# Kernel optimization log

Hardware: AMD Instinct MI355X
Metric: run time of the kernel (lower is better)

The kernel has to match this reference:

```python
import jax, jax.numpy as jnp
import numpy as np

B, N, D_MODEL, N_HEADS, WINDOW = 2, 2048, 1024, 16, 512
HEAD_DIM = D_MODEL // N_HEADS

def setup_inputs() -> dict:
    key = jax.random.key(0)
    k1, k2, k3 = jax.random.split(key, 3)
    x = jax.random.normal(k1, (B, N, D_MODEL), dtype=jnp.float32)
    W_qkv = jax.random.normal(k2, (D_MODEL, 3 * D_MODEL), dtype=jnp.float32) * 0.02
    W_proj = jax.random.normal(k3, (D_MODEL, D_MODEL), dtype=jnp.float32) * 0.02
    b_proj = jnp.zeros((D_MODEL,), dtype=jnp.float32)
    return {"x": x, "W_qkv": W_qkv, "W_proj": W_proj, "b_proj": b_proj}

def reference(x, W_qkv, W_proj, b_proj):
    Bx, Nx, C = x.shape
    H, Dh = N_HEADS, C // N_HEADS
    scale = Dh ** -0.5
    window = min(WINDOW, Nx)
    half = window // 2
    # qkv: [B,N,3C] -> [3,B,H,N,Dh]
    qkv = (x @ W_qkv).reshape(Bx, Nx, 3, H, Dh).transpose(2, 0, 3, 1, 4)
    q, k, v = qkv[0], qkv[1], qkv[2]
    # banded mask: allowed iff i-half <= j <= i+half
    i = jnp.arange(Nx)[:, None]
    j = jnp.arange(Nx)[None, :]
    allowed = jnp.abs(i - j) <= half  # [N,N] bool
    attn = jnp.einsum('bhqd,bhkd->bhqk', q, k) * scale
    attn = jnp.where(allowed[None, None], attn, -jnp.inf)
    attn = jax.nn.softmax(attn, axis=-1)
    out = jnp.einsum('bhqk,bhkd->bhqd', attn, v)
    out = out.transpose(0, 2, 1, 3).reshape(Bx, Nx, C)
    return out @ W_proj + b_proj
```

## Files before the change

### kernel.cpp

```cpp
#include <hip/hip_runtime.h>
#include <stdint.h>


typedef _Float16 f16x8 __attribute__((ext_vector_type(8)));
typedef _Float16 f16x4 __attribute__((ext_vector_type(4)));
typedef float    f32x4 __attribute__((ext_vector_type(4)));

#define MFMA16(a, b, c) __builtin_amdgcn_mfma_f32_16x16x32_f16((a), (b), (c), 0, 0, 0)

__device__ __forceinline__ void gload16(const void* g, void* l) {
  __builtin_amdgcn_global_load_lds(
      (const __attribute__((address_space(1))) void*)g,
      (__attribute__((address_space(3))) void*)l, 16, 0, 0);
}

__global__ __launch_bounds__(256) void prep(const float* __restrict__ x,
                                            const float* __restrict__ wqkv,
                                            const float* __restrict__ wproj,
                                            _Float16* __restrict__ Xb,
                                            _Float16* __restrict__ Wqt,
                                            _Float16* __restrict__ Wpt) {
  __shared__ float t[64][65];
  const int id = blockIdx.x, tid = threadIdx.x;
  if (id < 4096) {
    int i = (id * 256 + tid) * 4;
    float4 v = *(const float4*)(x + i);
    f16x4 h;
    h[0] = (_Float16)v.x; h[1] = (_Float16)v.y;
    h[2] = (_Float16)v.z; h[3] = (_Float16)v.w;
    *(f16x4*)(Xb + i) = h;
    return;
  }
  const float* in; _Float16* out; int N, bx, by;
  if (id < 4864) { int tt = id - 4096; in = wqkv; out = Wqt; N = 3072; bx = tt % 48; by = tt / 48; }
  else           { int tt = id - 4864; in = wproj; out = Wpt; N = 1024; bx = tt & 15; by = tt >> 4; }
  const int n0 = bx * 64, k0 = by * 64;
  {
    int j = tid & 63;
#pragma unroll
    for (int p = 0; p < 16; p++) {
      int i = p * 4 + (tid >> 6);
      t[i][j] = in[(size_t)(k0 + i) * N + n0 + j];
    }
  }
  __syncthreads();
  {
    int i = tid & 63;
#pragma unroll
    for (int p = 0; p < 16; p++) {
      int j = p * 4 + (tid >> 6);
      out[(size_t)(n0 + j) * 1024 + k0 + i] = (_Float16)t[i][j];
    }
  }
}

__global__ __launch_bounds__(256) void vtrans(const _Float16* __restrict__ V,
                                              _Float16* __restrict__ Vt) {
  __shared__ _Float16 t[64][66];
  const int tid = threadIdx.x;
  const int bh = blockIdx.y, n0 = blockIdx.x * 64;
  const _Float16* Vg = V + (size_t)bh * 131072;
  {
    int dh0 = (tid & 7) * 8;
#pragma unroll
    for (int p = 0; p < 2; p++) {
      int nl = p * 32 + (tid >> 3);
      f16x8 v = *(const f16x8*)(Vg + (size_t)(n0 + nl) * 64 + dh0);
#pragma unroll
      for (int e = 0; e < 8; e++) t[nl][dh0 + e] = v[e];
    }
  }
  __syncthreads();
  {
    int dh = tid >> 2, nb = (tid & 3) * 16;
    f16x8 a, b;
#pragma unroll
    for (int e = 0; e < 8; e++) { a[e] = t[nb + e][dh]; b[e] = t[nb + 8 + e][dh]; }
    _Float16* dst = Vt + (size_t)bh * 131072 + (size_t)dh * 2048 + n0 + nb;
    *(f16x8*)dst = a;
    *(f16x8*)(dst + 8) = b;
  }
}

template <int BM, int BN, int EPI>
__global__ __launch_bounds__(256) void gemm16(const _Float16* __restrict__ A,
                                              const _Float16* __restrict__ Bt,
                                              const int K,
                                              _Float16* __restrict__ oh,
                                              float* __restrict__ of,
                                              const float* __restrict__ bias,
                                              const int Nout) {
  constexpr int RF = BM / 32, CF = BN / 32;
  constexpr int SLABS = (BM + BN) / 8;
  __shared__ __align__(16) char smem[(BM + BN) * 128];
  char* As = smem;
  char* Bs = smem + BM * 128;
  const int tid = threadIdx.x, wave = tid >> 6, lane = tid & 63;
  const int il = lane & 15, ih = lane >> 4;
  const int bm = blockIdx.y * BM, bn = blockIdx.x * BN;
  const int wm = wave >> 1, wn = wave & 1;
  const int rs = lane >> 3, cp = lane & 7;

  f32x4 acc[RF][CF] = {};

  for (int k0 = 0; k0 < K; k0 += 64) {
    __syncthreads();
#pragma unroll
    for (int s0 = 0; s0 < SLABS / 4; s0++) {
      int s = wave + s0 * 4;
      int row = s * 8 + rs;
      int c = cp ^ (row & 7);
      if (row < BM)
        gload16(A + (size_t)(bm + row) * K + k0 + c * 8, As + s * 1024);
      else
        gload16(Bt + (size_t)(bn + row - BM) * K + k0 + c * 8, smem + s * 1024);
    }
    __syncthreads();
#pragma unroll
    for (int ks = 0; ks < 2; ks++) {
      f16x8 af[RF], bf[CF];
#pragma unroll
      for (int rf = 0; rf < RF; rf++) {
        int R = wm * (BM / 2) + rf * 16 + il;
        af[rf] = *(const f16x8*)(As + R * 128 + (((ks * 4 + ih) ^ (R & 7)) * 16));
      }
#pragma unroll
      for (int cf = 0; cf < CF; cf++) {
        int C = wn * (BN / 2) + cf * 16 + il;
        bf[cf] = *(const f16x8*)(Bs + C * 128 + (((ks * 4 + ih) ^ (C & 7)) * 16));
      }
#pragma unroll
      for (int rf = 0; rf < RF; rf++)
#pragma unroll
        for (int cf = 0; cf < CF; cf++)
          acc[rf][cf] = MFMA16(af[rf], bf[cf], acc[rf][cf]);
    }
  }

#pragma unroll
  for (int rf = 0; rf < RF; rf++)
#pragma unroll
    for (int cf = 0; cf < CF; cf++)
#pragma unroll
      for (int r = 0; r < 4; r++) {
        int row = bm + wm * (BM / 2) + rf * 16 + ih * 4 + r;
        int col = bn + wn * (BN / 2) + cf * 16 + il;
        float v = acc[rf][cf][r];
        if (EPI == 0) {
          int sec = col >> 10, cc = col & 1023;
          if (sec == 0) v *= 0.18033688f;
          size_t plane = (size_t)(sec * 32 + (row >> 11) * 16 + (cc >> 6));
          oh[plane * 131072 + (size_t)(row & 2047) * 64 + (cc & 63)] = (_Float16)v;
        } else {
          of[(size_t)row * Nout + col] = v + bias[col];
        }
      }
}

__global__ __launch_bounds__(512) void attn128(const _Float16* __restrict__ QKV,
                                               const _Float16* __restrict__ VT,
                                               _Float16* __restrict__ O2) {
  __shared__ __align__(16) char smem[49152];
  const int tid = threadIdx.x, wave = tid >> 6, lane = tid & 63;
  const int il = lane & 15, ih = lane >> 4;
  const int q0 = blockIdx.x * 128, bh = blockIdx.y;
  const _Float16* Qg = QKV + (size_t)bh * 131072;
  const _Float16* Kg = QKV + 4194304 + (size_t)bh * 131072;
  const _Float16* Vg = VT + (size_t)bh * 131072;

  const int t0 = (q0 >= 256) ? (q0 - 256) : 0;
  const int t1 = (q0 + 384 <= 2048) ? (q0 + 384) : 2048;
  const int niter = (t1 - t0) >> 6;

  const int rs = lane >> 3, cp = lane & 7;
#pragma unroll
  for (int q = 0; q < 2; q++) {
    int s = wave * 2 + q;
    int row = s * 8 + rs;
    int c = cp ^ (row & 7);
    gload16(Qg + (size_t)(q0 + row) * 64 + c * 8, smem + s * 1024);
  }
  {
    char* Kp = smem + 16384;
    int row = wave * 8 + rs;
    int c = cp ^ (row & 7);
    gload16(Kg + (size_t)(t0 + row) * 64 + c * 8, Kp + wave * 1024);
    gload16(Vg + (size_t)row * 2048 + t0 + c * 8, Kp + 8192 + wave * 1024);
  }
  __syncthreads();

  f16x8 aq[2];
#pragma unroll
  for (int ks = 0; ks < 2; ks++) {
    int row = wave * 16 + il;
    aq[ks] = *(const f16x8*)(smem + row * 128 + (((ks * 4 + ih) ^ (row & 7)) * 16));
  }

  char* Pw = smem + wave * 2048;
  f32x4 o[4] = {};
  float l_r[4] = {0.f, 0.f, 0.f, 0.f};
  const int a0 = q0 + wave * 16;

  for (int i = 0; i < niter; i++) {
    const int kt = t0 + i * 64;
    char* Kp = smem + 16384 + (i & 1) * 16384;
    char* Vp = Kp + 8192;
    if (i + 1 < niter) {
      char* Kn = smem + 16384 + ((i + 1) & 1) * 16384;
      int kt2 = kt + 64;
      int row = wave * 8 + rs;
      int c = cp ^ (row & 7);
      gload16(Kg + (size_t)(kt2 + row) * 64 + c * 8, Kn + wave * 1024);
      gload16(Vg + (size_t)row * 2048 + kt2 + c * 8, Kn + 8192 + wave * 1024);
    }

    bool outb[4];
    int d0s[4];
#pragma unroll
    for (int cf = 0; cf < 4; cf++) {
      int d0 = a0 - (kt + cf * 16);
      d0s[cf] = d0;
      outb[cf] = (d0 >= 272) || (d0 <= -272);
    }
#pragma unroll
    for (int cf = 0; cf < 4; cf++) {
      if (outb[cf]) {
        if (!outb[cf ^ 1]) {
#pragma unroll
          for (int r = 0; r < 4; r++) {
            int prow = ih * 4 + r;
            int key = cf * 16 + il;
            *(_Float16*)(Pw + prow * 128 + (((key >> 3) ^ (prow & 7)) * 16) +
                         (key & 7) * 2) = (_Float16)0.f;
          }
        }
        continue;
      }
      f32x4 s4 = {0.f, 0.f, 0.f, 0.f};
#pragma unroll
      for (int ks = 0; ks < 2; ks++) {
        int kr = cf * 16 + il;
        f16x8 bk = *(const f16x8*)(Kp + kr * 128 + (((ks * 4 + ih) ^ (kr & 7)) * 16));
        s4 = MFMA16(aq[ks], bk, s4);
      }
      const int d0 = d0s[cf];
#pragma unroll
      for (int r = 0; r < 4; r++) {
        float p = __builtin_amdgcn_exp2f(s4[r]);
        int qr = ih * 4 + r;
        if (d0 == 256) p = (qr <= il) ? p : 0.f;
        else if (d0 == -256) p = (qr >= il) ? p : 0.f;
        l_r[r] += p;
        int key = cf * 16 + il;
        *(_Float16*)(Pw + qr * 128 + (((key >> 3) ^ (qr & 7)) * 16) +
                     (key & 7) * 2) = (_Float16)p;
      }
    }
#pragma unroll
    for (int ks = 0; ks < 2; ks++) {
      if (outb[2 * ks] && outb[2 * ks + 1]) continue;
      f16x8 pa = *(const f16x8*)(Pw + il * 128 + (((ks * 4 + ih) ^ (il & 7)) * 16));
#pragma unroll
      for (int f = 0; f < 4; f++) {
        int dr = f * 16 + il;
        f16x8 vb = *(const f16x8*)(Vp + dr * 128 + (((ks * 4 + ih) ^ (dr & 7)) * 16));
        o[f] = MFMA16(pa, vb, o[f]);
      }
    }
    __syncthreads();
  }

  const int b = bh >> 4, h = bh & 15;
#pragma unroll
  for (int r = 0; r < 4; r++) {
    float l = l_r[r];
    l += __shfl_xor(l, 1);
    l += __shfl_xor(l, 2);
    l += __shfl_xor(l, 4);
    l += __shfl_xor(l, 8);
    float inv = 1.0f / l;
    int n = a0 + ih * 4 + r;
#pragma unroll
    for (int f = 0; f < 4; f++) {
      int col = h * 64 + f * 16 + il;
      O2[(size_t)(b * 2048 + n) * 1024 + col] = (_Float16)(o[f][r] * inv);
    }
  }
}


extern "C" void kernel_launch(void* const* d_in, const int* in_sizes, int n_in,
                              void* d_out, int out_size, void* d_ws, size_t ws_size,
                              hipStream_t stream) {
  const float* x = (const float*)d_in[0];
  const float* wqkv = (const float*)d_in[1];
  const float* wproj = (const float*)d_in[2];
  const float* bproj = (const float*)d_in[3];
  float* out = (float*)d_out;
  char* ws = (char*)d_ws;

  _Float16* Xb  = (_Float16*)(ws);
  _Float16* Wqt = (_Float16*)(ws + (size_t)(8  << 20));
  _Float16* Wpt = (_Float16*)(ws + (size_t)(14 << 20));
  _Float16* QKV = (_Float16*)(ws + (size_t)(16 << 20));
  _Float16* Vt  = (_Float16*)(ws + (size_t)(40 << 20));
  _Float16* O2  = (_Float16*)(ws);

  prep<<<5120, 256, 0, stream>>>(x, wqkv, wproj, Xb, Wqt, Wpt);
  gemm16<128, 128, 0><<<dim3(24, 32), 256, 0, stream>>>(Xb, Wqt, 1024, QKV, nullptr,
                                                        nullptr, 0);
  vtrans<<<dim3(32, 32), 256, 0, stream>>>(QKV + 8388608, Vt);
  attn128<<<dim3(16, 32), 512, 0, stream>>>(QKV, Vt, O2);
  gemm16<128, 128, 1><<<dim3(8, 32), 256, 0, stream>>>(O2, Wpt, 1024, nullptr, out,
                                                       bproj, 1024);
}
```

Before: 169.4 us.

## Restructure banded attention with 32x32 MFMA and split-key waves

The attention kernel now uses 32x32x16 MFMA tiles. Each pair of waves shares 32 query rows and splits each 128-key tile between them, and the two partial outputs are merged through shared memory at the end. K/V double buffering is replaced by a single 128-key buffer that is loaded after a barrier, trading prefetch overlap for fewer loop iterations and larger MFMA tiles. The output projection GEMM also switches to 128x64 tiles, doubling the block count to improve occupancy.

```diff
diff --git a/kernel.cpp b/kernel.cpp
--- a/kernel.cpp
+++ b/kernel.cpp
@@ -5,8 +5,10 @@
 typedef _Float16 f16x8 __attribute__((ext_vector_type(8)));
 typedef _Float16 f16x4 __attribute__((ext_vector_type(4)));
 typedef float    f32x4 __attribute__((ext_vector_type(4)));
+typedef float    f32x16 __attribute__((ext_vector_type(16)));
 
 #define MFMA16(a, b, c) __builtin_amdgcn_mfma_f32_16x16x32_f16((a), (b), (c), 0, 0, 0)
+#define MFMA32(a, b, c) __builtin_amdgcn_mfma_f32_32x32x16_f16((a), (b), (c), 0, 0, 0)
 
 __device__ __forceinline__ void gload16(const void* g, void* l) {
   __builtin_amdgcn_global_load_lds(
@@ -157,134 +159,155 @@
       }
 }
 
-__global__ __launch_bounds__(512) void attn128(const _Float16* __restrict__ QKV,
-                                               const _Float16* __restrict__ VT,
-                                               _Float16* __restrict__ O2) {
-  __shared__ __align__(16) char smem[49152];
+__global__ __launch_bounds__(512) void attn(const _Float16* __restrict__ QKV,
+                                            const _Float16* __restrict__ VT,
+                                            _Float16* __restrict__ O2) {
+  __shared__ __align__(16) char smem[65536];
+  char* Ks = smem + 32768;
+  char* Vs = smem + 49152;
   const int tid = threadIdx.x, wave = tid >> 6, lane = tid & 63;
-  const int il = lane & 15, ih = lane >> 4;
+  const int qw = wave >> 1, sh = wave & 1;
+  const int cl = lane & 31, hl = lane >> 5;
+  const int rs = lane >> 3, cp = lane & 7;
   const int q0 = blockIdx.x * 128, bh = blockIdx.y;
   const _Float16* Qg = QKV + (size_t)bh * 131072;
   const _Float16* Kg = QKV + 4194304 + (size_t)bh * 131072;
   const _Float16* Vg = VT + (size_t)bh * 131072;
-
-  const int t0 = (q0 >= 256) ? (q0 - 256) : 0;
-  const int t1 = (q0 + 384 <= 2048) ? (q0 + 384) : 2048;
-  const int niter = (t1 - t0) >> 6;
-
-  const int rs = lane >> 3, cp = lane & 7;
+  const int t0 = (q0 >= 256) ? q0 - 256 : 0;
+  const int t1 = (q0 + 384 <= 2048) ? q0 + 384 : 2048;
+  const int niter = (t1 - t0) >> 7;
+
 #pragma unroll
   for (int q = 0; q < 2; q++) {
-    int s = wave * 2 + q;
+    int s = 2 * wave + q;
     int row = s * 8 + rs;
     int c = cp ^ (row & 7);
     gload16(Qg + (size_t)(q0 + row) * 64 + c * 8, smem + s * 1024);
   }
-  {
-    char* Kp = smem + 16384;
-    int row = wave * 8 + rs;
-    int c = cp ^ (row & 7);
-    gload16(Kg + (size_t)(t0 + row) * 64 + c * 8, Kp + wave * 1024);
-    gload16(Vg + (size_t)row * 2048 + t0 + c * 8, Kp + 8192 + wave * 1024);
-  }
-  __syncthreads();
-
-  f16x8 aq[2];
-#pragma unroll
-  for (int ks = 0; ks < 2; ks++) {
-    int row = wave * 16 + il;
-    aq[ks] = *(const f16x8*)(smem + row * 128 + (((ks * 4 + ih) ^ (row & 7)) * 16));
-  }
-
-  char* Pw = smem + wave * 2048;
-  f32x4 o[4] = {};
-  float l_r[4] = {0.f, 0.f, 0.f, 0.f};
-  const int a0 = q0 + wave * 16;
+#pragma unroll
+  for (int q = 0; q < 2; q++) {
+    int s = 2 * wave + q;
+    int krow = s * 8 + rs;
+    int c = cp ^ (krow & 7);
+    gload16(Kg + (size_t)(t0 + krow) * 64 + c * 8, Ks + s * 1024);
+    int sub = s >> 3, vrow = (s & 7) * 8 + rs;
+    int cv = cp ^ (vrow & 7);
+    gload16(Vg + (size_t)vrow * 2048 + t0 + 64 * sub + cv * 8,
+            Vs + sub * 8192 + (s & 7) * 1024);
+  }
+  __syncthreads();
+  f16x8 bq[4];
+  {
+    int row = 32 * qw + cl;
+#pragma unroll
+    for (int ks = 0; ks < 4; ks++)
+      bq[ks] = *(const f16x8*)(smem + row * 128 + (((ks * 2 + hl) ^ (row & 7)) * 16));
+  }
+  __syncthreads();
+
+  char* Pw = smem + wave * 4096;
+  f32x16 oacc[2] = {};
+  float l_acc = 0.f;
+  const int a0 = q0 + 32 * qw;
 
   for (int i = 0; i < niter; i++) {
-    const int kt = t0 + i * 64;
-    char* Kp = smem + 16384 + (i & 1) * 16384;
-    char* Vp = Kp + 8192;
+    const int kt = t0 + i * 128;
+    const int d0a = a0 - (kt + 64 * sh);
+    const int d0b = d0a - 32;
+    const bool deadA = (d0a >= 288) || (d0a <= -288);
+    const bool deadB = (d0b >= 288) || (d0b <= -288);
+    if (!(deadA && deadB)) {
+#pragma unroll
+      for (int cb = 0; cb < 2; cb++) {
+        const int d0 = cb ? d0b : d0a;
+        const bool dead = cb ? deadB : deadA;
+        if (dead) {
+#pragma unroll
+          for (int g = 0; g < 4; g++) {
+            f16x4 z = {};
+            *(f16x4*)(Pw + cl * 128 + (((4 * cb + g) ^ (cl & 7)) * 16) + 8 * hl) = z;
+          }
+          continue;
+        }
+        f32x16 st = {};
+        const int krow = 64 * sh + 32 * cb + cl;
+#pragma unroll
+        for (int ks = 0; ks < 4; ks++) {
+          f16x8 ak = *(const f16x8*)(Ks + krow * 128 + (((ks * 2 + hl) ^ (krow & 7)) * 16));
+          st = MFMA32(ak, bq[ks], st);
+        }
+#pragma unroll
+        for (int g = 0; g < 4; g++) {
+          f16x4 hv;
+#pragma unroll
+          for (int i2 = 0; i2 < 4; i2++) {
+            float e = __builtin_amdgcn_exp2f(st[g * 4 + i2]);
+            int rowk = 8 * g + 4 * hl + i2;
+            if (d0 == 256) e = (cl <= rowk) ? e : 0.f;
+            else if (d0 == -256) e = (cl >= rowk) ? e : 0.f;
+            l_acc += e;
+            hv[i2] = (_Float16)e;
+          }
+          *(f16x4*)(Pw + cl * 128 + (((4 * cb + g) ^ (cl & 7)) * 16) + 8 * hl) = hv;
+        }
+      }
+      f16x8 bp[4];
+#pragma unroll
+      for (int ks = 0; ks < 4; ks++)
+        bp[ks] = *(const f16x8*)(Pw + cl * 128 + (((ks * 2 + hl) ^ (cl & 7)) * 16));
+#pragma unroll
+      for (int db = 0; db < 2; db++) {
+        const int vrow = 32 * db + cl;
+#pragma unroll
+        for (int ks = 0; ks < 4; ks++) {
+          f16x8 av = *(const f16x8*)(Vs + sh * 8192 + vrow * 128 +
+                                     (((ks * 2 + hl) ^ (vrow & 7)) * 16));
+          oacc[db] = MFMA32(av, bp[ks], oacc[db]);
+        }
+      }
+    }
+    __syncthreads();
     if (i + 1 < niter) {
-      char* Kn = smem + 16384 + ((i + 1) & 1) * 16384;
-      int kt2 = kt + 64;
-      int row = wave * 8 + rs;
-      int c = cp ^ (row & 7);
-      gload16(Kg + (size_t)(kt2 + row) * 64 + c * 8, Kn + wave * 1024);
-      gload16(Vg + (size_t)row * 2048 + kt2 + c * 8, Kn + 8192 + wave * 1024);
-    }
-
-    bool outb[4];
-    int d0s[4];
-#pragma unroll
-    for (int cf = 0; cf < 4; cf++) {
-      int d0 = a0 - (kt + cf * 16);
-      d0s[cf] = d0;
-      outb[cf] = (d0 >= 272) || (d0 <= -272);
-    }
-#pragma unroll
-    for (int cf = 0; cf < 4; cf++) {
-      if (outb[cf]) {
-        if (!outb[cf ^ 1]) {
-#pragma unroll
-          for (int r = 0; r < 4; r++) {
-            int prow = ih * 4 + r;
-            int key = cf * 16 + il;
-            *(_Float16*)(Pw + prow * 128 + (((key >> 3) ^ (prow & 7)) * 16) +
-                         (key & 7) * 2) = (_Float16)0.f;
-          }
-        }
-        continue;
-      }
-      f32x4 s4 = {0.f, 0.f, 0.f, 0.f};
-#pragma unroll
-      for (int ks = 0; ks < 2; ks++) {
-        int kr = cf * 16 + il;
-        f16x8 bk = *(const f16x8*)(Kp + kr * 128 + (((ks * 4 + ih) ^ (kr & 7)) * 16));
-        s4 = MFMA16(aq[ks], bk, s4);
-      }
-      const int d0 = d0s[cf];
-#pragma unroll
-      for (int r = 0; r < 4; r++) {
-        float p = __builtin_amdgcn_exp2f(s4[r]);
-        int qr = ih * 4 + r;
-        if (d0 == 256) p = (qr <= il) ? p : 0.f;
-        else if (d0 == -256) p = (qr >= il) ? p : 0.f;
-        l_r[r] += p;
-        int key = cf * 16 + il;
-        *(_Float16*)(Pw + qr * 128 + (((key >> 3) ^ (qr & 7)) * 16) +
-                     (key & 7) * 2) = (_Float16)p;
-      }
-    }
-#pragma unroll
-    for (int ks = 0; ks < 2; ks++) {
-      if (outb[2 * ks] && outb[2 * ks + 1]) continue;
-      f16x8 pa = *(const f16x8*)(Pw + il * 128 + (((ks * 4 + ih) ^ (il & 7)) * 16));
-#pragma unroll
-      for (int f = 0; f < 4; f++) {
-        int dr = f * 16 + il;
-        f16x8 vb = *(const f16x8*)(Vp + dr * 128 + (((ks * 4 + ih) ^ (dr & 7)) * 16));
-        o[f] = MFMA16(pa, vb, o[f]);
+      const int kt2 = kt + 128;
+#pragma unroll
+      for (int q = 0; q < 2; q++) {
+        int s = 2 * wave + q;
+        int krow = s * 8 + rs;
+        int c = cp ^ (krow & 7);
+        gload16(Kg + (size_t)(kt2 + krow) * 64 + c * 8, Ks + s * 1024);
+        int sub = s >> 3, vrow = (s & 7) * 8 + rs;
+        int cv = cp ^ (vrow & 7);
+        gload16(Vg + (size_t)vrow * 2048 + kt2 + 64 * sub + cv * 8,
+                Vs + sub * 8192 + (s & 7) * 1024);
       }
     }
     __syncthreads();
   }
 
-  const int b = bh >> 4, h = bh & 15;
-#pragma unroll
-  for (int r = 0; r < 4; r++) {
-    float l = l_r[r];
-    l += __shfl_xor(l, 1);
-    l += __shfl_xor(l, 2);
-    l += __shfl_xor(l, 4);
-    l += __shfl_xor(l, 8);
-    float inv = 1.0f / l;
-    int n = a0 + ih * 4 + r;
-#pragma unroll
-    for (int f = 0; f < 4; f++) {
-      int col = h * 64 + f * 16 + il;
-      O2[(size_t)(b * 2048 + n) * 1024 + col] = (_Float16)(o[f][r] * inv);
-    }
+  l_acc += __shfl_xor(l_acc, 32);
+  float* ov = (float*)oacc;
+  if (sh == 1) {
+#pragma unroll
+    for (int r = 0; r < 8; r++)
+      *(f32x4*)(smem + qw * 8192 + lane * 128 + r * 16) = *(const f32x4*)(ov + r * 4);
+    *(float*)(smem + 32768 + qw * 128 + cl * 4) = l_acc;
+  }
+  __syncthreads();
+  if (sh == 0) {
+    float inv = 1.0f / (l_acc + *(const float*)(smem + 32768 + qw * 128 + cl * 4));
+    const int b = bh >> 4, h = bh & 15;
+    _Float16* dst = O2 + (size_t)(b * 2048 + q0 + 32 * qw + cl) * 1024 + h * 64;
+#pragma unroll
+    for (int db = 0; db < 2; db++)
+#pragma unroll
+      for (int g = 0; g < 4; g++) {
+        f32x4 po = *(const f32x4*)(smem + qw * 8192 + lane * 128 + (db * 4 + g) * 16);
+        f16x4 hv;
+#pragma unroll
+        for (int i2 = 0; i2 < 4; i2++)
+          hv[i2] = (_Float16)((ov[db * 16 + g * 4 + i2] + po[i2]) * inv);
+        *(f16x4*)(dst + 32 * db + 8 * g + 4 * hl) = hv;
+      }
   }
 }
 
@@ -310,7 +333,7 @@
   gemm16<128, 128, 0><<<dim3(24, 32), 256, 0, stream>>>(Xb, Wqt, 1024, QKV, nullptr,
                                                         nullptr, 0);
   vtrans<<<dim3(32, 32), 256, 0, stream>>>(QKV + 8388608, Vt);
-  attn128<<<dim3(16, 32), 512, 0, stream>>>(QKV, Vt, O2);
-  gemm16<128, 128, 1><<<dim3(8, 32), 256, 0, stream>>>(O2, Wpt, 1024, nullptr, out,
+  attn<<<dim3(16, 32), 512, 0, stream>>>(QKV, Vt, O2);
+  gemm16<128, 64, 1><<<dim3(16, 32), 256, 0, stream>>>(O2, Wpt, 1024, nullptr, out,
                                                        bproj, 1024);
 }
```

Measured after the change: 167.2 us. Within noise of the previous version (-1.3%).
